# Performance work log

Measured on AMD Instinct MI355X. Metric: run time of the kernel, lower is better.

Reference implementation:

```python
import jax, jax.numpy as jnp
import numpy as np

D_MODEL = 1024
H = 16
D_K = D_MODEL // H
D_FF = 4096
EPS = 1e-6
NEG = -1e9


def setup_inputs() -> dict:
    key = jax.random.key(0)
    ks = jax.random.split(key, 8)
    B, S = 2, 2048
    src = jax.random.normal(ks[0], (B, S, D_MODEL), dtype=jnp.float32)
    src_mask = jnp.ones((B, 1, 1, S), dtype=jnp.int32)
    sc = 1.0 / np.sqrt(D_MODEL)
    wq = jax.random.normal(ks[1], (D_MODEL, D_MODEL), jnp.float32) * sc
    wk = jax.random.normal(ks[2], (D_MODEL, D_MODEL), jnp.float32) * sc
    wv = jax.random.normal(ks[3], (D_MODEL, D_MODEL), jnp.float32) * sc
    wo = jax.random.normal(ks[4], (D_MODEL, D_MODEL), jnp.float32) * sc
    w1 = jax.random.normal(ks[5], (D_FF, D_MODEL), jnp.float32) * sc
    b1 = jnp.zeros((D_FF,), jnp.float32)
    w2 = jax.random.normal(ks[6], (D_MODEL, D_FF), jnp.float32) * (1.0 / np.sqrt(D_FF))
    b2 = jnp.zeros((D_MODEL,), jnp.float32)
    a1 = jnp.ones((1,), jnp.float32)
    be1 = jnp.zeros((1,), jnp.float32)
    a2 = jnp.ones((1,), jnp.float32)
    be2 = jnp.zeros((1,), jnp.float32)
    return dict(src=src, src_mask=src_mask, wq=wq, wk=wk, wv=wv, wo=wo,
                w1=w1, b1=b1, w2=w2, b2=b2, a1=a1, be1=be1, a2=a2, be2=be2)


def layer_norm(x, alpha, bias):
    # torch: mean + unbiased std (ddof=1), eps added to std
    mean = jnp.mean(x, axis=-1, keepdims=True)
    std = jnp.sqrt(jnp.var(x, axis=-1, keepdims=True, ddof=1))
    return alpha * (x - mean) / (std + EPS) + bias


def mha(x, mask, wq, wk, wv, wo):
    B, S, _ = x.shape
    def split(t):  # [B,S,D] -> [B,H,S,D_K]
        return t.reshape(B, S, H, D_K).transpose(0, 2, 1, 3)
    q = split(x @ wq.T)
    k = split(x @ wk.T)
    v = split(x @ wv.T)
    scores = jnp.einsum('bhqd,bhkd->bhqk', q, k) / np.sqrt(D_K)
    scores = jnp.where(mask == 0, NEG, scores)
    attn = jax.nn.softmax(scores, axis=-1)
    out = jnp.einsum('bhqk,bhkd->bhqd', attn, v)
    out = out.transpose(0, 2, 1, 3).reshape(B, S, D_MODEL)
    return out @ wo.T


def reference(src, src_mask, wq, wk, wv, wo, w1, b1, w2, b2, a1, be1, a2, be2):
    x = layer_norm(src, a1, be1)
    src = src + mha(x, src_mask, wq, wk, wv, wo)
    x = layer_norm(src, a2, be2)
    ff = jax.nn.relu(x @ w1.T + b1) @ w2.T + b2
    return src + ff
```

## Files before the change

kernel.cpp:

```cpp
#include <hip/hip_runtime.h>
#include <hip/hip_bf16.h>

typedef unsigned short u16;
typedef unsigned int u32;
typedef float floatx4 __attribute__((ext_vector_type(4)));
typedef __bf16 bf16x8 __attribute__((ext_vector_type(8)));
typedef u16 ushort4v __attribute__((ext_vector_type(4)));
typedef u16 ushort8v __attribute__((ext_vector_type(8)));

#define DEVI static __device__ __forceinline__

DEVI u16 f2bf(float f) {
    u32 u = __builtin_bit_cast(u32, f);
    u += 0x7fffu + ((u >> 16) & 1u);
    return (u16)(u >> 16);
}

DEVI float fexp2(float x) { return __builtin_amdgcn_exp2f(x); }

DEVI void async_cp16(const u16* g, u16* l) {
    __builtin_amdgcn_global_load_lds((const __attribute__((address_space(1))) u32*)g,
                                     (__attribute__((address_space(3))) u32*)l, 16, 0, 0);
}

template<int C> DEVI float dppf(float x) {
    return __builtin_bit_cast(float,
        __builtin_amdgcn_update_dpp(0, __builtin_bit_cast(int, x), C, 0xf, 0xf, true));
}
DEVI float rsum16(float v) {
    v += dppf<0x121>(v); v += dppf<0x122>(v);
    v += dppf<0x124>(v); v += dppf<0x128>(v); return v;
}

template<int BM, int BN, int RW, int CW, bool QKV3, bool SPLITK,
         bool BIAS, bool RELU, bool RESID, bool OBF16>
__global__ __launch_bounds__(256) void gemm_nt(
    const u16* __restrict__ A,
    const u16* __restrict__ W0, const u16* __restrict__ W1, const u16* __restrict__ W2,
    const float* __restrict__ bias, const float* __restrict__ resid,
    void* __restrict__ o0, void* __restrict__ o1, void* __restrict__ o2,
    int K, int lda, int Nper, int NX)
{
    static_assert(RW * CW == 4, "4 waves");
    constexpr int WM = BM / RW, WN = BN / CW;
    constexpr int MI = WM / 16, NI = WN / 16;
    __shared__ __align__(16) u16 As[2][BM * 32];
    __shared__ __align__(16) u16 Bs[2][BN * 32];
    const int tid = threadIdx.x;
    const int w = tid >> 6, lane = tid & 63;
    const int q = lane >> 4, ml = lane & 15;
    const int wr = w / CW, wc = w % CW;
    const int m0 = blockIdx.y * BM;
    int bx = blockIdx.x;
    size_t kbase = 0;
    int half = 0;
    if (SPLITK) { half = bx / NX; bx -= half * NX; kbase = (size_t)half * K; }
    int n0 = bx * BN;
    const u16* W = W0;
    void* outp = o0;
    if (QKV3) {
        int sel = n0 / Nper;
        n0 -= sel * Nper;
        W = (sel == 0) ? W0 : (sel == 1 ? W1 : W2);
        outp = (sel == 0) ? o0 : (sel == 1 ? o1 : o2);
    }
    if (SPLITK) outp = half ? o1 : o0;

    auto stage = [&](int buf, int kt) {
#pragma unroll
        for (int p = 0; p < BM / 64; ++p) {
            int g = p * 256 + tid;
            int r = g >> 2, s = g & 3;
            int c = s ^ ((r >> 1) & 3);
            async_cp16(A + (size_t)(m0 + r) * lda + kbase + kt + c * 8,
                       &As[buf][(p * 256 + w * 64) * 8]);
        }
#pragma unroll
        for (int p = 0; p < BN / 64; ++p) {
            int g = p * 256 + tid;
            int r = g >> 2, s = g & 3;
            int c = s ^ ((r >> 1) & 3);
            async_cp16(W + (size_t)(n0 + r) * lda + kbase + kt + c * 8,
                       &Bs[buf][(p * 256 + w * 64) * 8]);
        }
    };

    const floatx4 fzero = {0.f, 0.f, 0.f, 0.f};
    floatx4 acc[MI][NI];
#pragma unroll
    for (int i = 0; i < MI; ++i)
#pragma unroll
        for (int j = 0; j < NI; ++j) acc[i][j] = fzero;

    stage(0, 0);
    for (int it = 0, kt = 0; kt < K; ++it, kt += 32) {
        __syncthreads();
        if (kt + 32 < K) stage((it + 1) & 1, kt + 32);
        const u16* Asb = As[it & 1];
        const u16* Bsb = Bs[it & 1];
        bf16x8 af[MI], bfr[NI];
#pragma unroll
        for (int i = 0; i < MI; ++i) {
            int rm = wr * WM + i * 16 + ml;
            int s = q ^ ((rm >> 1) & 3);
            af[i] = *(const bf16x8*)&Asb[(rm * 4 + s) * 8];
        }
#pragma unroll
        for (int j = 0; j < NI; ++j) {
            int rn = wc * WN + j * 16 + ml;
            int s = q ^ ((rn >> 1) & 3);
            bfr[j] = *(const bf16x8*)&Bsb[(rn * 4 + s) * 8];
        }
#pragma unroll
        for (int i = 0; i < MI; ++i)
#pragma unroll
            for (int j = 0; j < NI; ++j)
                acc[i][j] = __builtin_amdgcn_mfma_f32_16x16x32_bf16(af[i], bfr[j], acc[i][j], 0, 0, 0);
    }

#pragma unroll
    for (int j = 0; j < NI; ++j) {
        int gn = n0 + wc * WN + j * 16 + ml;
        float bj = 0.f;
        if (BIAS) bj = bias[gn];
#pragma unroll
        for (int i = 0; i < MI; ++i) {
            int gm0 = m0 + wr * WM + i * 16 + q * 4;
#pragma unroll
            for (int r = 0; r < 4; ++r) {
                size_t idx = (size_t)(gm0 + r) * Nper + gn;
                float v = acc[i][j][r] + bj;
                if (RELU) v = fmaxf(v, 0.f);
                if (RESID) v += resid[idx];
                if (OBF16) ((u16*)outp)[idx] = f2bf(v);
                else       ((float*)outp)[idx] = v;
            }
        }
    }
}

__global__ __launch_bounds__(256, 4) void flash4(
    const u16* __restrict__ Q, const u16* __restrict__ Kg,
    const u16* __restrict__ Vt, const float* __restrict__ biasv,
    u16* __restrict__ O)
{
    __shared__ __align__(16) u16 Ks[2][64 * 64];
    __shared__ __align__(16) u16 Vs[2][64 * 64];
    __shared__ __align__(16) u16 Ps[4][16 * 64];
    const int tid = threadIdx.x;
    const int w = tid >> 6, lane = tid & 63;
    const int q = lane >> 4, ml = lane & 15;
    const int b = blockIdx.y >> 4, h = blockIdx.y & 15;
    const size_t rowQ = (size_t)(b * 2048 + blockIdx.x * 64);
    const float KSC = 0.125f * 1.4426950408889634f;
    const floatx4 fzero = {0.f, 0.f, 0.f, 0.f};

    bf16x8 qa[2];
#pragma unroll
    for (int c = 0; c < 2; ++c)
        qa[c] = *(const bf16x8*)&Q[(rowQ + w * 16 + ml) * 1024 + h * 64 + q * 8 + c * 32];

    auto stage = [&](int buf, int s0) {
#pragma unroll
        for (int p = 0; p < 2; ++p) {
            int L = p * 256 + tid;
            int row = L >> 3, sl = L & 7;
            int ch = sl ^ (row & 7);
            async_cp16(Kg + (size_t)(b * 2048 + s0 + row) * 1024 + h * 64 + ch * 8,
                       &Ks[buf][(p * 256 + w * 64) * 8]);
            async_cp16(Vt + (size_t)(b * 1024 + h * 64 + row) * 2048 + s0 + ch * 8,
                       &Vs[buf][(p * 256 + w * 64) * 8]);
        }
    };

    floatx4 oacc[4];
    float lsum[4];
#pragma unroll
    for (int d = 0; d < 4; ++d) oacc[d] = fzero;
#pragma unroll
    for (int r = 0; r < 4; ++r) lsum[r] = 0.f;

    stage(0, 0);
    for (int it = 0; it < 32; ++it) {
        __syncthreads();
        if (it + 1 < 32) stage((it + 1) & 1, (it + 1) * 64);
        const u16* Kb = Ks[it & 1];
        const u16* Vb = Vs[it & 1];
        const int s0 = it * 64;

        float bf[4];
#pragma unroll
        for (int cf = 0; cf < 4; ++cf) bf[cf] = biasv[b * 2048 + s0 + cf * 16 + ml];

#pragma unroll
        for (int cf = 0; cf < 4; ++cf) {
            int krow = cf * 16 + ml;
            bf16x8 k0 = *(const bf16x8*)&Kb[krow * 64 + ((q + 0) ^ (krow & 7)) * 8];
            bf16x8 k1 = *(const bf16x8*)&Kb[krow * 64 + ((q + 4) ^ (krow & 7)) * 8];
            floatx4 t = fzero;
            t = __builtin_amdgcn_mfma_f32_16x16x32_bf16(qa[0], k0, t, 0, 0, 0);
            t = __builtin_amdgcn_mfma_f32_16x16x32_bf16(qa[1], k1, t, 0, 0, 0);
#pragma unroll
            for (int r = 0; r < 4; ++r) {
                float p = fexp2(fmaf(t[r], KSC, bf[cf]));
                lsum[r] += p;
                u32 u = __builtin_bit_cast(u32, p) + 0x8000u;
                int prow = q * 4 + r;
                int sl = (cf * 2 + (ml >> 3)) ^ (prow & 7);
                Ps[w][prow * 64 + sl * 8 + (ml & 7)] = (u16)(u >> 16);
            }
        }
        asm volatile("s_waitcnt lgkmcnt(0)" ::: "memory");
        bf16x8 pa[2];
#pragma unroll
        for (int c = 0; c < 2; ++c)
            pa[c] = *(const bf16x8*)&Ps[w][ml * 64 + ((q + 4 * c) ^ (ml & 7)) * 8];
#pragma unroll
        for (int d = 0; d < 4; ++d) {
            int vrow = d * 16 + ml;
            bf16x8 v0 = *(const bf16x8*)&Vb[vrow * 64 + ((q + 0) ^ (vrow & 7)) * 8];
            bf16x8 v1 = *(const bf16x8*)&Vb[vrow * 64 + ((q + 4) ^ (vrow & 7)) * 8];
            oacc[d] = __builtin_amdgcn_mfma_f32_16x16x32_bf16(pa[0], v0, oacc[d], 0, 0, 0);
            oacc[d] = __builtin_amdgcn_mfma_f32_16x16x32_bf16(pa[1], v1, oacc[d], 0, 0, 0);
        }
    }
#pragma unroll
    for (int r = 0; r < 4; ++r) {
        float rcp = 1.f / rsum16(lsum[r]);
        size_t row = rowQ + w * 16 + q * 4 + r;
#pragma unroll
        for (int d = 0; d < 4; ++d)
            O[row * 1024 + h * 64 + d * 16 + ml] = f2bf(oacc[d][r] * rcp);
    }
}

__global__ __launch_bounds__(256) void vtrans(const u16* __restrict__ Vb, u16* __restrict__ Vt)
{
    __shared__ __align__(16) u16 T[64 * 72];
    const int tid = threadIdx.x;
    const int ct = blockIdx.x, rt = blockIdx.y;
    const int b = rt >> 5;
    const int s0 = (rt & 31) * 64;
    const int c0 = ct * 64;
#pragma unroll
    for (int p = 0; p < 2; ++p) {
        int slot = p * 256 + tid;
        int lr = slot >> 3, pc = slot & 7;
        bf16x8 v = *(const bf16x8*)&Vb[(size_t)(b * 2048 + s0 + lr) * 1024 + c0 + pc * 8];
        *(bf16x8*)&T[lr * 72 + pc * 8] = v;
    }
    __syncthreads();
#pragma unroll
    for (int p = 0; p < 2; ++p) {
        int slot = p * 256 + tid;
        int dc = slot >> 3, sc0 = (slot & 7) * 8;
        ushort8v o;
#pragma unroll
        for (int j = 0; j < 8; ++j) o[j] = T[(sc0 + j) * 72 + dc];
        *(ushort8v*)&Vt[(size_t)(b * 1024 + c0 + dc) * 2048 + s0 + sc0] = o;
    }
}

__global__ __launch_bounds__(256) void ln_bf16(const float* __restrict__ x,
    const float* __restrict__ ga, const float* __restrict__ gb, u16* __restrict__ y)
{
    const int row = blockIdx.x, tid = threadIdx.x;
    const float4 v = ((const float4*)(x + (size_t)row * 1024))[tid];
    float s = v.x + v.y + v.z + v.w;
    float ss = v.x * v.x + v.y * v.y + v.z * v.z + v.w * v.w;
#pragma unroll
    for (int d = 1; d < 64; d <<= 1) { s += __shfl_xor(s, d, 64); ss += __shfl_xor(ss, d, 64); }
    __shared__ float ps[4], pss[4];
    const int w = tid >> 6, lane = tid & 63;
    if (lane == 0) { ps[w] = s; pss[w] = ss; }
    __syncthreads();
    s = ps[0] + ps[1] + ps[2] + ps[3];
    ss = pss[0] + pss[1] + pss[2] + pss[3];
    float mean = s * (1.f / 1024.f);
    float var = fmaxf((ss - s * mean) * (1.f / 1023.f), 0.f);
    float sc = ga[0] / (sqrtf(var) + 1e-6f);
    float bb = gb[0];
    ushort4v o;
    o[0] = f2bf((v.x - mean) * sc + bb);
    o[1] = f2bf((v.y - mean) * sc + bb);
    o[2] = f2bf((v.z - mean) * sc + bb);
    o[3] = f2bf((v.w - mean) * sc + bb);
    ((ushort4v*)(y + (size_t)row * 1024))[tid] = o;
}

__global__ __launch_bounds__(256) void cast_all(
    const float* __restrict__ wq, const float* __restrict__ wk,
    const float* __restrict__ wv, const float* __restrict__ wo,
    const float* __restrict__ w1, const float* __restrict__ w2,
    u16* __restrict__ wqb, u16* __restrict__ wkb, u16* __restrict__ wvb,
    u16* __restrict__ wob, u16* __restrict__ w1b, u16* __restrict__ w2b)
{
    size_t i = (size_t)blockIdx.x * 256 + threadIdx.x;
    const float* s; u16* d; size_t off;
    if (i < 262144)       { s = wq; d = wqb; off = i; }
    else if (i < 524288)  { s = wk; d = wkb; off = i - 262144; }
    else if (i < 786432)  { s = wv; d = wvb; off = i - 524288; }
    else if (i < 1048576) { s = wo; d = wob; off = i - 786432; }
    else if (i < 2097152) { s = w1; d = w1b; off = i - 1048576; }
    else                  { s = w2; d = w2b; off = i - 2097152; }
    float4 v = ((const float4*)s)[off];
    ushort4v o = {f2bf(v.x), f2bf(v.y), f2bf(v.z), f2bf(v.w)};
    ((ushort4v*)d)[off] = o;
}

__global__ __launch_bounds__(256) void mask_bias(const int* __restrict__ m, float* __restrict__ bias)
{
    int i = blockIdx.x * 256 + threadIdx.x;
    if (i < 4096) bias[i] = m[i] ? 0.f : -1.442695e9f;
}

__global__ __launch_bounds__(256) void ff2_fin(const float* __restrict__ p0, const float* __restrict__ p1,
    const float* __restrict__ b2, const float* __restrict__ resid, float* __restrict__ out)
{
    const size_t i = (size_t)blockIdx.x * 256 + threadIdx.x;
    float4 a = ((const float4*)p0)[i];
    float4 b = ((const float4*)p1)[i];
    float4 r = ((const float4*)resid)[i];
    float4 bb = ((const float4*)b2)[i & 255];
    float4 o = {a.x + b.x + r.x + bb.x, a.y + b.y + r.y + bb.y,
                a.z + b.z + r.z + bb.z, a.w + b.w + r.w + bb.w};
    ((float4*)out)[i] = o;
}

extern "C" void kernel_launch(void* const* d_in, const int* in_sizes, int n_in,
                              void* d_out, int out_size, void* d_ws, size_t ws_size,
                              hipStream_t stream)
{
    const float* src = (const float*)d_in[0];
    const int* msk   = (const int*)d_in[1];
    const float* wq  = (const float*)d_in[2];
    const float* wk  = (const float*)d_in[3];
    const float* wv  = (const float*)d_in[4];
    const float* wo  = (const float*)d_in[5];
    const float* w1  = (const float*)d_in[6];
    const float* b1  = (const float*)d_in[7];
    const float* w2  = (const float*)d_in[8];
    const float* b2  = (const float*)d_in[9];
    const float* a1  = (const float*)d_in[10];
    const float* be1 = (const float*)d_in[11];
    const float* a2  = (const float*)d_in[12];
    const float* be2 = (const float*)d_in[13];
    float* out = (float*)d_out;

    char* ws = (char*)d_ws;
    const size_t MB = (size_t)1 << 20;
    u16* wqb  = (u16*)(ws + 0 * MB);
    u16* wkb  = (u16*)(ws + 2 * MB);
    u16* wvb  = (u16*)(ws + 4 * MB);
    u16* wob  = (u16*)(ws + 6 * MB);
    u16* w1b  = (u16*)(ws + 8 * MB);
    u16* w2b  = (u16*)(ws + 16 * MB);
    u16* xln1 = (u16*)(ws + 24 * MB);
    u16* attn = xln1;
    u16* Qb   = (u16*)(ws + 32 * MB);
    u16* xln2 = Qb;
    u16* Kb   = (u16*)(ws + 40 * MB);
    u16* Vb   = (u16*)(ws + 48 * MB);
    u16* Vt   = (u16*)(ws + 56 * MB);
    float* biasv = (float*)(ws + 64 * MB);
    u16* h1   = (u16*)(ws + 40 * MB);
    float* src2 = (float*)(ws + 72 * MB);
    float* P0 = (float*)(ws + 0 * MB);
    float* P1 = (float*)(ws + 24 * MB);

    cast_all<<<12288, 256, 0, stream>>>(wq, wk, wv, wo, w1, w2,
                                        wqb, wkb, wvb, wob, w1b, w2b);
    mask_bias<<<16, 256, 0, stream>>>(msk, biasv);

    ln_bf16<<<4096, 256, 0, stream>>>(src, a1, be1, xln1);

    gemm_nt<128, 128, 2, 2, true, false, false, false, false, true><<<dim3(24, 32), 256, 0, stream>>>(
        xln1, wqb, wkb, wvb, nullptr, nullptr, Qb, Kb, Vb, 1024, 1024, 1024, 0);

    vtrans<<<dim3(16, 64), 256, 0, stream>>>(Vb, Vt);

    flash4<<<dim3(32, 32), 256, 0, stream>>>(Qb, Kb, Vt, biasv, attn);

    gemm_nt<128, 64, 4, 1, false, false, false, false, true, false><<<dim3(16, 32), 256, 0, stream>>>(
        attn, wob, nullptr, nullptr, nullptr, src, src2, nullptr, nullptr, 1024, 1024, 1024, 0);

    ln_bf16<<<4096, 256, 0, stream>>>(src2, a2, be2, xln2);

    gemm_nt<128, 128, 2, 2, false, false, true, true, false, true><<<dim3(32, 32), 256, 0, stream>>>(
        xln2, w1b, nullptr, nullptr, b1, nullptr, h1, nullptr, nullptr, 1024, 1024, 4096, 0);

    gemm_nt<128, 128, 2, 2, false, true, false, false, false, false><<<dim3(16, 32), 256, 0, stream>>>(
        h1, w2b, nullptr, nullptr, nullptr, nullptr, P0, P1, nullptr, 2048, 4096, 1024, 8);

    ff2_fin<<<4096, 256, 0, stream>>>(P0, P1, b2, src2, out);
}
```

Before: 367.1 us.

## Keep attention probabilities in registers via transposed S=K·Qᵀ MFMA layout

The flash attention kernel now computes the score tile transposed (K as the A operand, Q as B), so each lane's MFMA output already matches the B-operand layout of a 16x16x16 bf16 MFMA. The probabilities are packed to bf16 in registers and fed straight into the PV product, which removes the per-wave LDS round trip for P and its waitcnt. The row-sum reduction becomes two cross-lane shuffles and the output stores are packed pairs. In exchange, PV uses twice as many smaller-K MFMAs with narrower 8-byte V reads from LDS.

After: 382.2 us. 1.04x slower.

```diff
diff --git a/kernel.cpp b/kernel.cpp
--- a/kernel.cpp
+++ b/kernel.cpp
@@ -5,8 +5,10 @@
 typedef unsigned int u32;
 typedef float floatx4 __attribute__((ext_vector_type(4)));
 typedef __bf16 bf16x8 __attribute__((ext_vector_type(8)));
+typedef __bf16 bf16x4 __attribute__((ext_vector_type(4)));
 typedef u16 ushort4v __attribute__((ext_vector_type(4)));
 typedef u16 ushort8v __attribute__((ext_vector_type(8)));
+typedef short short4v __attribute__((ext_vector_type(4)));
 
 #define DEVI static __device__ __forceinline__
 
@@ -18,18 +20,22 @@
 
 DEVI float fexp2(float x) { return __builtin_amdgcn_exp2f(x); }
 
+DEVI floatx4 mfma16(bf16x4 a, bf16x4 b, floatx4 c) {
+#if __has_builtin(__builtin_amdgcn_mfma_f32_16x16x16_bf16)
+    return __builtin_amdgcn_mfma_f32_16x16x16_bf16(a, b, c, 0, 0, 0);
+#elif __has_builtin(__builtin_amdgcn_mfma_f32_16x16x16bf16_1k)
+    return __builtin_amdgcn_mfma_f32_16x16x16bf16_1k(
+        __builtin_bit_cast(short4v, a), __builtin_bit_cast(short4v, b), c, 0, 0, 0);
+#else
+    floatx4 d = c;
+    asm("v_mfma_f32_16x16x16_bf16 %0, %1, %2, %0" : "+v"(d) : "v"(a), "v"(b));
+    return d;
+#endif
+}
+
 DEVI void async_cp16(const u16* g, u16* l) {
     __builtin_amdgcn_global_load_lds((const __attribute__((address_space(1))) u32*)g,
                                      (__attribute__((address_space(3))) u32*)l, 16, 0, 0);
-}
-
-template<int C> DEVI float dppf(float x) {
-    return __builtin_bit_cast(float,
-        __builtin_amdgcn_update_dpp(0, __builtin_bit_cast(int, x), C, 0xf, 0xf, true));
-}
-DEVI float rsum16(float v) {
-    v += dppf<0x121>(v); v += dppf<0x122>(v);
-    v += dppf<0x124>(v); v += dppf<0x128>(v); return v;
 }
 
 template<int BM, int BN, int RW, int CW, bool QKV3, bool SPLITK,
@@ -139,14 +145,13 @@
     }
 }
 
-__global__ __launch_bounds__(256, 4) void flash4(
+__global__ __launch_bounds__(256, 4) void flash5(
     const u16* __restrict__ Q, const u16* __restrict__ Kg,
     const u16* __restrict__ Vt, const float* __restrict__ biasv,
     u16* __restrict__ O)
 {
     __shared__ __align__(16) u16 Ks[2][64 * 64];
     __shared__ __align__(16) u16 Vs[2][64 * 64];
-    __shared__ __align__(16) u16 Ps[4][16 * 64];
     const int tid = threadIdx.x;
     const int w = tid >> 6, lane = tid & 63;
     const int q = lane >> 4, ml = lane & 15;
@@ -174,11 +179,9 @@
     };
 
     floatx4 oacc[4];
-    float lsum[4];
+    float lsum = 0.f;
 #pragma unroll
     for (int d = 0; d < 4; ++d) oacc[d] = fzero;
-#pragma unroll
-    for (int r = 0; r < 4; ++r) lsum[r] = 0.f;
 
     stage(0, 0);
     for (int it = 0; it < 32; ++it) {
@@ -188,50 +191,51 @@
         const u16* Vb = Vs[it & 1];
         const int s0 = it * 64;
 
-        float bf[4];
-#pragma unroll
-        for (int cf = 0; cf < 4; ++cf) bf[cf] = biasv[b * 2048 + s0 + cf * 16 + ml];
-
+        bf16x4 pfrag[4];
 #pragma unroll
         for (int cf = 0; cf < 4; ++cf) {
             int krow = cf * 16 + ml;
             bf16x8 k0 = *(const bf16x8*)&Kb[krow * 64 + ((q + 0) ^ (krow & 7)) * 8];
             bf16x8 k1 = *(const bf16x8*)&Kb[krow * 64 + ((q + 4) ^ (krow & 7)) * 8];
             floatx4 t = fzero;
-            t = __builtin_amdgcn_mfma_f32_16x16x32_bf16(qa[0], k0, t, 0, 0, 0);
-            t = __builtin_amdgcn_mfma_f32_16x16x32_bf16(qa[1], k1, t, 0, 0, 0);
-#pragma unroll
-            for (int r = 0; r < 4; ++r) {
-                float p = fexp2(fmaf(t[r], KSC, bf[cf]));
-                lsum[r] += p;
-                u32 u = __builtin_bit_cast(u32, p) + 0x8000u;
-                int prow = q * 4 + r;
-                int sl = (cf * 2 + (ml >> 3)) ^ (prow & 7);
-                Ps[w][prow * 64 + sl * 8 + (ml & 7)] = (u16)(u >> 16);
+            t = __builtin_amdgcn_mfma_f32_16x16x32_bf16(k0, qa[0], t, 0, 0, 0);
+            t = __builtin_amdgcn_mfma_f32_16x16x32_bf16(k1, qa[1], t, 0, 0, 0);
+            const float4 bb = *(const float4*)&biasv[b * 2048 + s0 + cf * 16 + q * 4];
+            float p0 = fexp2(fmaf(t[0], KSC, bb.x));
+            float p1 = fexp2(fmaf(t[1], KSC, bb.y));
+            float p2 = fexp2(fmaf(t[2], KSC, bb.z));
+            float p3 = fexp2(fmaf(t[3], KSC, bb.w));
+            lsum += (p0 + p1) + (p2 + p3);
+            u32 lo01 = (__builtin_bit_cast(u32, p0) + 0x8000u) >> 16;
+            u32 hi01 = (__builtin_bit_cast(u32, p1) + 0x8000u) & 0xffff0000u;
+            u32 lo23 = (__builtin_bit_cast(u32, p2) + 0x8000u) >> 16;
+            u32 hi23 = (__builtin_bit_cast(u32, p3) + 0x8000u) & 0xffff0000u;
+            u32 pk[2] = {lo01 | hi01, lo23 | hi23};
+            pfrag[cf] = __builtin_bit_cast(bf16x4, *(ulong1*)pk);
+        }
+#pragma unroll
+        for (int dt = 0; dt < 4; ++dt) {
+            int vrow = dt * 16 + ml;
+#pragma unroll
+            for (int cf = 0; cf < 4; ++cf) {
+                int sl = (cf * 2 + (q >> 1)) ^ (vrow & 7);
+                bf16x4 vf = *(const bf16x4*)&Vb[vrow * 64 + sl * 8 + (q & 1) * 4];
+                oacc[dt] = mfma16(vf, pfrag[cf], oacc[dt]);
             }
         }
-        asm volatile("s_waitcnt lgkmcnt(0)" ::: "memory");
-        bf16x8 pa[2];
-#pragma unroll
-        for (int c = 0; c < 2; ++c)
-            pa[c] = *(const bf16x8*)&Ps[w][ml * 64 + ((q + 4 * c) ^ (ml & 7)) * 8];
-#pragma unroll
-        for (int d = 0; d < 4; ++d) {
-            int vrow = d * 16 + ml;
-            bf16x8 v0 = *(const bf16x8*)&Vb[vrow * 64 + ((q + 0) ^ (vrow & 7)) * 8];
-            bf16x8 v1 = *(const bf16x8*)&Vb[vrow * 64 + ((q + 4) ^ (vrow & 7)) * 8];
-            oacc[d] = __builtin_amdgcn_mfma_f32_16x16x32_bf16(pa[0], v0, oacc[d], 0, 0, 0);
-            oacc[d] = __builtin_amdgcn_mfma_f32_16x16x32_bf16(pa[1], v1, oacc[d], 0, 0, 0);
-        }
-    }
-#pragma unroll
-    for (int r = 0; r < 4; ++r) {
-        float rcp = 1.f / rsum16(lsum[r]);
-        size_t row = rowQ + w * 16 + q * 4 + r;
-#pragma unroll
-        for (int d = 0; d < 4; ++d)
-            O[row * 1024 + h * 64 + d * 16 + ml] = f2bf(oacc[d][r] * rcp);
-    }
+    }
+    lsum += __shfl_xor(lsum, 16, 64);
+    lsum += __shfl_xor(lsum, 32, 64);
+    const float rcp = 1.f / lsum;
+    const size_t row = rowQ + w * 16 + ml;
+#pragma unroll
+    for (int dt = 0; dt < 4; ++dt)
+#pragma unroll
+        for (int rp = 0; rp < 4; rp += 2) {
+            u32 pk = (u32)f2bf(oacc[dt][rp] * rcp)
+                   | ((u32)f2bf(oacc[dt][rp + 1] * rcp) << 16);
+            *(u32*)&O[row * 1024 + h * 64 + dt * 16 + q * 4 + rp] = pk;
+        }
 }
 
 __global__ __launch_bounds__(256) void vtrans(const u16* __restrict__ Vb, u16* __restrict__ Vt)
@@ -379,7 +383,7 @@
 
     vtrans<<<dim3(16, 64), 256, 0, stream>>>(Vb, Vt);
 
-    flash4<<<dim3(32, 32), 256, 0, stream>>>(Qb, Kb, Vt, biasv, attn);
+    flash5<<<dim3(32, 32), 256, 0, stream>>>(Qb, Kb, Vt, biasv, attn);
 
     gemm_nt<128, 64, 4, 1, false, false, false, false, true, false><<<dim3(16, 32), 256, 0, stream>>>(
         attn, wob, nullptr, nullptr, nullptr, src, src2, nullptr, nullptr, 1024, 1024, 1024, 0);
```

## Keep softmax probabilities in registers via transposed QK MFMA in flash kernel

Applied to the files above, without the earlier changes.

The attention kernel now computes S^T (K as the A operand, Q as B) so each lane's MFMA output directly forms a bf16 P fragment for the PV MFMA. This removes the LDS round-trip for P. Each wave now handles 32 query rows instead of 16, so every K/V fragment read from LDS is reused across two query groups. Blocks shrink to 128 threads with a new swizzle matching the permuted K row order. Fewer waves per block and more registers per wave may reduce occupancy and latency hiding.

New measurement: 365.2 us. No clear change (-0.5%).

```diff
diff --git a/kernel.cpp b/kernel.cpp
--- a/kernel.cpp
+++ b/kernel.cpp
@@ -21,15 +21,6 @@
 DEVI void async_cp16(const u16* g, u16* l) {
     __builtin_amdgcn_global_load_lds((const __attribute__((address_space(1))) u32*)g,
                                      (__attribute__((address_space(3))) u32*)l, 16, 0, 0);
-}
-
-template<int C> DEVI float dppf(float x) {
-    return __builtin_bit_cast(float,
-        __builtin_amdgcn_update_dpp(0, __builtin_bit_cast(int, x), C, 0xf, 0xf, true));
-}
-DEVI float rsum16(float v) {
-    v += dppf<0x121>(v); v += dppf<0x122>(v);
-    v += dppf<0x124>(v); v += dppf<0x128>(v); return v;
 }
 
 template<int BM, int BN, int RW, int CW, bool QKV3, bool SPLITK,
@@ -139,14 +130,13 @@
     }
 }
 
-__global__ __launch_bounds__(256, 4) void flash4(
+__global__ __launch_bounds__(128, 2) void flash7(
     const u16* __restrict__ Q, const u16* __restrict__ Kg,
     const u16* __restrict__ Vt, const float* __restrict__ biasv,
     u16* __restrict__ O)
 {
     __shared__ __align__(16) u16 Ks[2][64 * 64];
     __shared__ __align__(16) u16 Vs[2][64 * 64];
-    __shared__ __align__(16) u16 Ps[4][16 * 64];
     const int tid = threadIdx.x;
     const int w = tid >> 6, lane = tid & 63;
     const int q = lane >> 4, ml = lane & 15;
@@ -155,30 +145,36 @@
     const float KSC = 0.125f * 1.4426950408889634f;
     const floatx4 fzero = {0.f, 0.f, 0.f, 0.f};
 
-    bf16x8 qa[2];
-#pragma unroll
-    for (int c = 0; c < 2; ++c)
-        qa[c] = *(const bf16x8*)&Q[(rowQ + w * 16 + ml) * 1024 + h * 64 + q * 8 + c * 32];
+    bf16x8 qa[2][2];
+#pragma unroll
+    for (int qg = 0; qg < 2; ++qg)
+#pragma unroll
+        for (int c = 0; c < 2; ++c)
+            qa[qg][c] = *(const bf16x8*)&Q[(rowQ + w * 32 + qg * 16 + ml) * 1024
+                                           + h * 64 + q * 8 + c * 32];
 
     auto stage = [&](int buf, int s0) {
 #pragma unroll
-        for (int p = 0; p < 2; ++p) {
-            int L = p * 256 + tid;
+        for (int p = 0; p < 4; ++p) {
+            int L = p * 128 + tid;
             int row = L >> 3, sl = L & 7;
-            int ch = sl ^ (row & 7);
+            int ch = sl ^ ((row & 3) | (((row >> 3) & 1) << 2));
             async_cp16(Kg + (size_t)(b * 2048 + s0 + row) * 1024 + h * 64 + ch * 8,
-                       &Ks[buf][(p * 256 + w * 64) * 8]);
+                       &Ks[buf][(p * 128 + w * 64) * 8]);
             async_cp16(Vt + (size_t)(b * 1024 + h * 64 + row) * 2048 + s0 + ch * 8,
-                       &Vs[buf][(p * 256 + w * 64) * 8]);
+                       &Vs[buf][(p * 128 + w * 64) * 8]);
         }
     };
 
-    floatx4 oacc[4];
-    float lsum[4];
-#pragma unroll
-    for (int d = 0; d < 4; ++d) oacc[d] = fzero;
-#pragma unroll
-    for (int r = 0; r < 4; ++r) lsum[r] = 0.f;
+    floatx4 oacc[2][4];
+    float lsum[2] = {0.f, 0.f};
+#pragma unroll
+    for (int qg = 0; qg < 2; ++qg)
+#pragma unroll
+        for (int d = 0; d < 4; ++d) oacc[qg][d] = fzero;
+
+    const int swk = (ml & 3) | (((ml >> 2) & 1) << 2);
+    const int swv = (ml & 3) | (((ml >> 3) & 1) << 2);
 
     stage(0, 0);
     for (int it = 0; it < 32; ++it) {
@@ -188,49 +184,72 @@
         const u16* Vb = Vs[it & 1];
         const int s0 = it * 64;
 
-        float bf[4];
-#pragma unroll
-        for (int cf = 0; cf < 4; ++cf) bf[cf] = biasv[b * 2048 + s0 + cf * 16 + ml];
-
-#pragma unroll
-        for (int cf = 0; cf < 4; ++cf) {
-            int krow = cf * 16 + ml;
-            bf16x8 k0 = *(const bf16x8*)&Kb[krow * 64 + ((q + 0) ^ (krow & 7)) * 8];
-            bf16x8 k1 = *(const bf16x8*)&Kb[krow * 64 + ((q + 4) ^ (krow & 7)) * 8];
-            floatx4 t = fzero;
-            t = __builtin_amdgcn_mfma_f32_16x16x32_bf16(qa[0], k0, t, 0, 0, 0);
-            t = __builtin_amdgcn_mfma_f32_16x16x32_bf16(qa[1], k1, t, 0, 0, 0);
-#pragma unroll
-            for (int r = 0; r < 4; ++r) {
-                float p = fexp2(fmaf(t[r], KSC, bf[cf]));
-                lsum[r] += p;
-                u32 u = __builtin_bit_cast(u32, p) + 0x8000u;
-                int prow = q * 4 + r;
-                int sl = (cf * 2 + (ml >> 3)) ^ (prow & 7);
-                Ps[w][prow * 64 + sl * 8 + (ml & 7)] = (u16)(u >> 16);
+        bf16x8 pfrag[2][2];
+#pragma unroll
+        for (int g = 0; g < 2; ++g) {
+            const int re = g * 32 + ((ml >> 2) << 3) + (ml & 3);
+            bf16x8 ke0 = *(const bf16x8*)&Kb[(re + 0) * 64 + ((0 + q) ^ swk) * 8];
+            bf16x8 ke1 = *(const bf16x8*)&Kb[(re + 0) * 64 + ((4 + q) ^ swk) * 8];
+            bf16x8 ko0 = *(const bf16x8*)&Kb[(re + 4) * 64 + ((0 + q) ^ swk) * 8];
+            bf16x8 ko1 = *(const bf16x8*)&Kb[(re + 4) * 64 + ((4 + q) ^ swk) * 8];
+            const float4 be = *(const float4*)&biasv[b * 2048 + s0 + g * 32 + q * 8];
+            const float4 bo = *(const float4*)&biasv[b * 2048 + s0 + g * 32 + q * 8 + 4];
+#pragma unroll
+            for (int qg = 0; qg < 2; ++qg) {
+                floatx4 te = fzero, to = fzero;
+                te = __builtin_amdgcn_mfma_f32_16x16x32_bf16(ke0, qa[qg][0], te, 0, 0, 0);
+                te = __builtin_amdgcn_mfma_f32_16x16x32_bf16(ke1, qa[qg][1], te, 0, 0, 0);
+                to = __builtin_amdgcn_mfma_f32_16x16x32_bf16(ko0, qa[qg][0], to, 0, 0, 0);
+                to = __builtin_amdgcn_mfma_f32_16x16x32_bf16(ko1, qa[qg][1], to, 0, 0, 0);
+                float pe0 = fexp2(fmaf(te[0], KSC, be.x));
+                float pe1 = fexp2(fmaf(te[1], KSC, be.y));
+                float pe2 = fexp2(fmaf(te[2], KSC, be.z));
+                float pe3 = fexp2(fmaf(te[3], KSC, be.w));
+                float po0 = fexp2(fmaf(to[0], KSC, bo.x));
+                float po1 = fexp2(fmaf(to[1], KSC, bo.y));
+                float po2 = fexp2(fmaf(to[2], KSC, bo.z));
+                float po3 = fexp2(fmaf(to[3], KSC, bo.w));
+                lsum[qg] += ((pe0 + pe1) + (pe2 + pe3)) + ((po0 + po1) + (po2 + po3));
+                u32 pk[4];
+                pk[0] = ((__builtin_bit_cast(u32, pe0) + 0x8000u) >> 16)
+                      | ((__builtin_bit_cast(u32, pe1) + 0x8000u) & 0xffff0000u);
+                pk[1] = ((__builtin_bit_cast(u32, pe2) + 0x8000u) >> 16)
+                      | ((__builtin_bit_cast(u32, pe3) + 0x8000u) & 0xffff0000u);
+                pk[2] = ((__builtin_bit_cast(u32, po0) + 0x8000u) >> 16)
+                      | ((__builtin_bit_cast(u32, po1) + 0x8000u) & 0xffff0000u);
+                pk[3] = ((__builtin_bit_cast(u32, po2) + 0x8000u) >> 16)
+                      | ((__builtin_bit_cast(u32, po3) + 0x8000u) & 0xffff0000u);
+                pfrag[g][qg] = __builtin_bit_cast(bf16x8, *(uint4*)pk);
             }
         }
-        asm volatile("s_waitcnt lgkmcnt(0)" ::: "memory");
-        bf16x8 pa[2];
-#pragma unroll
-        for (int c = 0; c < 2; ++c)
-            pa[c] = *(const bf16x8*)&Ps[w][ml * 64 + ((q + 4 * c) ^ (ml & 7)) * 8];
-#pragma unroll
-        for (int d = 0; d < 4; ++d) {
-            int vrow = d * 16 + ml;
-            bf16x8 v0 = *(const bf16x8*)&Vb[vrow * 64 + ((q + 0) ^ (vrow & 7)) * 8];
-            bf16x8 v1 = *(const bf16x8*)&Vb[vrow * 64 + ((q + 4) ^ (vrow & 7)) * 8];
-            oacc[d] = __builtin_amdgcn_mfma_f32_16x16x32_bf16(pa[0], v0, oacc[d], 0, 0, 0);
-            oacc[d] = __builtin_amdgcn_mfma_f32_16x16x32_bf16(pa[1], v1, oacc[d], 0, 0, 0);
-        }
-    }
-#pragma unroll
-    for (int r = 0; r < 4; ++r) {
-        float rcp = 1.f / rsum16(lsum[r]);
-        size_t row = rowQ + w * 16 + q * 4 + r;
-#pragma unroll
-        for (int d = 0; d < 4; ++d)
-            O[row * 1024 + h * 64 + d * 16 + ml] = f2bf(oacc[d][r] * rcp);
+#pragma unroll
+        for (int dt = 0; dt < 4; ++dt) {
+            int vrow = dt * 16 + ml;
+#pragma unroll
+            for (int g = 0; g < 2; ++g) {
+                bf16x8 vf = *(const bf16x8*)&Vb[vrow * 64 + ((g * 4 + q) ^ swv) * 8];
+#pragma unroll
+                for (int qg = 0; qg < 2; ++qg)
+                    oacc[qg][dt] = __builtin_amdgcn_mfma_f32_16x16x32_bf16(
+                        vf, pfrag[g][qg], oacc[qg][dt], 0, 0, 0);
+            }
+        }
+    }
+#pragma unroll
+    for (int qg = 0; qg < 2; ++qg) {
+        float ls = lsum[qg];
+        ls += __shfl_xor(ls, 16, 64);
+        ls += __shfl_xor(ls, 32, 64);
+        const float rcp = 1.f / ls;
+        const size_t row = rowQ + w * 32 + qg * 16 + ml;
+#pragma unroll
+        for (int dt = 0; dt < 4; ++dt)
+#pragma unroll
+            for (int rp = 0; rp < 4; rp += 2) {
+                u32 pk = (u32)f2bf(oacc[qg][dt][rp] * rcp)
+                       | ((u32)f2bf(oacc[qg][dt][rp + 1] * rcp) << 16);
+                *(u32*)&O[row * 1024 + h * 64 + dt * 16 + q * 4 + rp] = pk;
+            }
     }
 }
 
@@ -379,7 +398,7 @@
 
     vtrans<<<dim3(16, 64), 256, 0, stream>>>(Vb, Vt);
 
-    flash4<<<dim3(32, 32), 256, 0, stream>>>(Qb, Kb, Vt, biasv, attn);
+    flash7<<<dim3(32, 32), 128, 0, stream>>>(Qb, Kb, Vt, biasv, attn);
 
     gemm_nt<128, 64, 4, 1, false, false, false, false, true, false><<<dim3(16, 32), 256, 0, stream>>>(
         attn, wob, nullptr, nullptr, nullptr, src, src2, nullptr, nullptr, 1024, 1024, 1024, 0);
```
